# Kernel tuning notes

Measured on AMD Instinct MI355X. Metric: run time of the kernel, lower is better.

## Reference

```python
import jax, jax.numpy as jnp
import numpy as np

N = 100000      # nodes
E = 1600000     # edges (before self-loops)
FIN = 128       # in_channels
HID = 16        # hidden_channels
H = 8           # heads (layer 1)
OUT = 64        # out_channels
LN_EPS = 1e-5


def setup_inputs() -> dict:
    key = jax.random.key(0)
    ks = jax.random.split(key, 24)
    def p(i, shape):
        return jax.random.normal(ks[i], shape, dtype=jnp.float32) * 0.05
    return {
        "x": jax.random.normal(ks[0], (N, FIN), dtype=jnp.float32),
        "edge_index": jax.random.randint(ks[1], (2, E), 0, N, dtype=jnp.int32),
        # GATv2 layer 1: in -> H*HID, concat
        "Wl1": p(2, (FIN, H * HID)), "bl1": p(3, (H * HID,)),
        "Wr1": p(4, (FIN, H * HID)), "br1": p(5, (H * HID,)),
        "att1": p(6, (H, HID)), "bias1": p(7, (H * HID,)),
        # GATv2 layer 2: H*HID -> HID, heads=1
        "Wl2": p(8, (H * HID, HID)), "bl2": p(9, (HID,)),
        "Wr2": p(10, (H * HID, HID)), "br2": p(11, (HID,)),
        "att2": p(12, (1, HID)), "bias2": p(13, (HID,)),
        # LayerNorms
        "ln1_g": jnp.ones((H * HID,), jnp.float32), "ln1_b": jnp.zeros((H * HID,), jnp.float32),
        "ln2_g": jnp.ones((HID,), jnp.float32), "ln2_b": jnp.zeros((HID,), jnp.float32),
        # residual / skip / output linears
        "res1_W": p(14, (FIN, H * HID)), "res1_b": p(15, (H * HID,)),
        "res2_W": p(16, (H * HID, HID)), "res2_b": p(17, (HID,)),
        "skip_W": p(18, (H * HID, HID)), "skip_b": p(19, (HID,)),
        "out_W": p(20, (HID, OUT)), "out_b": p(21, (OUT,)),
    }


def _layernorm(x, g, b):
    mu = jnp.mean(x, axis=-1, keepdims=True)
    var = jnp.mean((x - mu) ** 2, axis=-1, keepdims=True)
    return (x - mu) * jax.lax.rsqrt(var + LN_EPS) * g + b


def _gatv2(x, src, dst, Wl, bl, Wr, br, att, bias, concat):
    # PyG GATv2Conv (share_weights=False, eval mode): message from src j to dst i
    Hh, C = att.shape
    n = x.shape[0]
    xl = (x @ Wl + bl).reshape(n, Hh, C)   # source-side transform
    xr = (x @ Wr + br).reshape(n, Hh, C)   # target-side transform
    m = xl[src] + xr[dst]                  # [E, H, C]
    e = jax.nn.leaky_relu(m, 0.2)
    alpha = jnp.einsum('ehc,hc->eh', e, att)          # [E, H]
    amax = jax.ops.segment_max(alpha, dst, num_segments=n)
    alpha = jnp.exp(alpha - amax[dst])
    denom = jax.ops.segment_sum(alpha, dst, num_segments=n)
    alpha = alpha / (denom[dst] + 1e-16)
    out = jax.ops.segment_sum(xl[src] * alpha[:, :, None], dst, num_segments=n)  # [N, H, C]
    out = out.reshape(n, Hh * C) if concat else out.mean(axis=1)
    return out + bias


def reference(x, edge_index, Wl1, bl1, Wr1, br1, att1, bias1,
              Wl2, bl2, Wr2, br2, att2, bias2,
              ln1_g, ln1_b, ln2_g, ln2_b,
              res1_W, res1_b, res2_W, res2_b, skip_W, skip_b, out_W, out_b):
    n = x.shape[0]
    loops = jnp.arange(n, dtype=edge_index.dtype)
    src = jnp.concatenate([edge_index[0], loops])
    dst = jnp.concatenate([edge_index[1], loops])

    h = _gatv2(x, src, dst, Wl1, bl1, Wr1, br1, att1, bias1, concat=True)
    h = _layernorm(h, ln1_g, ln1_b)
    h = h + (x @ res1_W + res1_b)
    h = jax.nn.elu(h)            # dropout off in eval

    skip_in = h
    h2 = _gatv2(h, src, dst, Wl2, bl2, Wr2, br2, att2, bias2, concat=False)
    h2 = _layernorm(h2, ln2_g, ln2_b)
    h2 = h2 + (skip_in @ res2_W + res2_b)
    h2 = jax.nn.elu(h2)
    h2 = h2 + (skip_in @ skip_W + skip_b)
    return h2 @ out_W + out_b
```

## Files before the change

kernel.cpp:

```cpp
#include <hip/hip_runtime.h>

typedef __attribute__((ext_vector_type(8))) short bf16x8;
typedef __attribute__((ext_vector_type(4))) float f32x4;

__device__ __forceinline__ float bf2f(ushort u) {
  union { uint i; float f; } v; v.i = ((uint)u) << 16; return v.f;
}
__device__ __forceinline__ ushort f2bf(float f) {
  union { float f; uint i; } v; v.f = f;
  uint r = (v.i + 0x7FFFu + ((v.i >> 16) & 1u)) >> 16;
  return (ushort)r;
}


__global__ __launch_bounds__(256) void k_zero(int* p, int n) {
  int i = blockIdx.x * 256 + threadIdx.x;
  if (i < n) p[i] = 0;
}

__global__ __launch_bounds__(256) void k_hist(const int* __restrict__ ei, int* __restrict__ cnt, int E) {
  int e = blockIdx.x * 256 + threadIdx.x;
  if (e < E) atomicAdd(&cnt[ei[E + e]], 1);
}

__global__ __launch_bounds__(256) void k_scan1(const int* __restrict__ cnt, int* __restrict__ partial, int n) {
  int i = blockIdx.x * 256 + threadIdx.x;
  int v = (i < n) ? cnt[i] : 0;
  #pragma unroll
  for (int m = 1; m < 64; m <<= 1) v += __shfl_xor(v, m);
  __shared__ int sm[4];
  if ((threadIdx.x & 63) == 0) sm[threadIdx.x >> 6] = v;
  __syncthreads();
  if (threadIdx.x == 0) partial[blockIdx.x] = sm[0] + sm[1] + sm[2] + sm[3];
}

__global__ __launch_bounds__(512) void k_scan2(int* partial, int nb) {
  __shared__ int buf[2][512];
  int t = threadIdx.x;
  int v = (t < nb) ? partial[t] : 0;
  buf[0][t] = v;
  __syncthreads();
  int cur = 0;
  for (int off = 1; off < 512; off <<= 1) {
    int x = buf[cur][t];
    if (t >= off) x += buf[cur][t - off];
    buf[cur ^ 1][t] = x;
    __syncthreads();
    cur ^= 1;
  }
  if (t < nb) partial[t] = buf[cur][t] - v;
}

__global__ __launch_bounds__(256) void k_scan3(const int* __restrict__ cnt, const int* __restrict__ partial,
                                               int* __restrict__ rowptr, int* __restrict__ cursor, int n) {
  __shared__ int buf[2][256];
  int t = threadIdx.x;
  int i = blockIdx.x * 256 + t;
  int v = (i < n) ? cnt[i] : 0;
  buf[0][t] = v;
  __syncthreads();
  int cur = 0;
  for (int off = 1; off < 256; off <<= 1) {
    int x = buf[cur][t];
    if (t >= off) x += buf[cur][t - off];
    buf[cur ^ 1][t] = x;
    __syncthreads();
    cur ^= 1;
  }
  if (i < n) {
    int incl = buf[cur][t];
    int base = partial[blockIdx.x];
    int rp = base + incl - v;
    rowptr[i] = rp;
    cursor[i] = rp;
    if (i == n - 1) rowptr[n] = base + incl;
  }
}

__global__ __launch_bounds__(256) void k_scatter(const int* __restrict__ ei, int* __restrict__ cursor,
                                                 int* __restrict__ ssrc, int E, int NS) {
  int t = threadIdx.x;
  int base = blockIdx.x * 2048;
  int src[8], dst[8];
  #pragma unroll
  for (int j = 0; j < 8; ++j) {
    int idx = base + j * 256 + t;
    bool ok = idx < E;
    src[j] = ok ? ei[idx] : 0;
    dst[j] = ok ? ei[E + idx] : -1;
  }
  for (int s = 0; s < NS; ++s) {
    #pragma unroll
    for (int j = 0; j < 8; ++j) {
      if ((dst[j] >> 13) == s) {
        int pos = atomicAdd(&cursor[dst[j]], 1);
        ssrc[pos] = src[j];
      }
    }
  }
}


__global__ __launch_bounds__(256) void k_conv(const float* __restrict__ x, ushort* __restrict__ AF, int total) {
  int t = blockIdx.x * 256 + threadIdx.x;
  if (t >= total) return;
  int m = t >> 4, k8 = t & 15;
  const float* src = x + (size_t)m * 128 + k8 * 8;
  float4 f0 = *(const float4*)src;
  float4 f1 = *(const float4*)(src + 4);
  uint4 o;
  o.x = f2bf(f0.x) | ((uint)f2bf(f0.y) << 16);
  o.y = f2bf(f0.z) | ((uint)f2bf(f0.w) << 16);
  o.z = f2bf(f1.x) | ((uint)f2bf(f1.y) << 16);
  o.w = f2bf(f1.z) | ((uint)f2bf(f1.w) << 16);
  size_t off = ((size_t)(((m >> 4) * 4 + (k8 >> 2)) * 64) + (m & 15) + ((k8 & 3) << 4)) * 8;
  *(uint4*)(AF + off) = o;
}


__global__ __launch_bounds__(256) void k_pack(
    const float* __restrict__ Wl1, const float* __restrict__ bl1,
    const float* __restrict__ Wr1, const float* __restrict__ br1,
    const float* __restrict__ res1W, const float* __restrict__ res1b,
    const float* __restrict__ Wl2, const float* __restrict__ bl2,
    const float* __restrict__ Wr2, const float* __restrict__ br2,
    const float* __restrict__ res2W, const float* __restrict__ res2b,
    const float* __restrict__ skipW, const float* __restrict__ skipb,
    ushort* __restrict__ W1F, float* __restrict__ B1P,
    ushort* __restrict__ W2F, float* __restrict__ B2P) {
  int tid = blockIdx.x * 256 + threadIdx.x;
  if (tid < 49152) {
    int j = tid & 7, l = (tid >> 3) & 63, ktile = (tid >> 9) & 3, ct = tid >> 11;
    int k = ktile * 32 + ((l >> 4) << 3) + j;
    int n = ct * 16 + (l & 15);
    int sel = n >> 7, jj = n & 127;
    const float* s = sel == 0 ? Wl1 : sel == 1 ? Wr1 : res1W;
    W1F[tid] = f2bf(s[k * 128 + jj]);
  } else if (tid < 57344) {
    int u = tid - 49152;
    int j = u & 7, l = (u >> 3) & 63, ktile = (u >> 9) & 3, ct = u >> 11;
    int k = ktile * 32 + ((l >> 4) << 3) + j;
    int n = ct * 16 + (l & 15);
    int sel = n >> 4, jj = n & 15;
    const float* s = sel == 0 ? Wl2 : sel == 1 ? Wr2 : sel == 2 ? res2W : skipW;
    W2F[u] = f2bf(s[k * 16 + jj]);
  } else if (tid < 57728) {
    int n = tid - 57344;
    int sel = n >> 7, jj = n & 127;
    const float* sb = sel == 0 ? bl1 : sel == 1 ? br1 : res1b;
    B1P[n] = sb[jj];
  } else if (tid < 57792) {
    int n = tid - 57728;
    int sel = n >> 4, jj = n & 15;
    const float* sb = sel == 0 ? bl2 : sel == 1 ? br2 : sel == 2 ? res2b : skipb;
    B2P[n] = sb[jj];
  }
}


__global__ __launch_bounds__(256) void k_mfma(
    const ushort* __restrict__ AF, const ushort* __restrict__ WF,
    const float* __restrict__ bias, ushort* __restrict__ C, int M, int P) {
  int w = threadIdx.x >> 6, l = threadIdx.x & 63;
  int m0 = blockIdx.x * 64;
  int c0 = blockIdx.y * 64 + w * 16;
  int ct = c0 >> 4;
  f32x4 acc[4] = {};
  #pragma unroll
  for (int kt = 0; kt < 4; ++kt) {
    bf16x8 b = *(const bf16x8*)(WF + ((size_t)((ct * 4 + kt) * 64 + l)) * 8);
    #pragma unroll
    for (int rt = 0; rt < 4; ++rt) {
      bf16x8 a = *(const bf16x8*)(AF + ((size_t)((blockIdx.x * 16 + rt * 4 + kt) * 64 + l)) * 8);
      acc[rt] = __builtin_amdgcn_mfma_f32_16x16x32_bf16(a, b, acc[rt], 0, 0, 0);
    }
  }
  int col = c0 + (l & 15);
  float bv = bias[col];
  int rbase = m0 + ((l >> 4) << 2);
  #pragma unroll
  for (int rt = 0; rt < 4; ++rt) {
    #pragma unroll
    for (int r = 0; r < 4; ++r) {
      int m = rbase + rt * 16 + r;
      if (m < M) C[(size_t)m * P + col] = f2bf(acc[rt][r] + bv);
    }
  }
}


__device__ __forceinline__ float2 ld2bf(const ushort* p) {
  uint u = *(const uint*)p;
  return make_float2(bf2f((ushort)u), bf2f((ushort)(u >> 16)));
}

#define EDGE1(v)                                            \
  {                                                         \
    float mx = (v).x + xr.x, my = (v).y + xr.y;             \
    mx = mx > 0.f ? mx : 0.2f * mx;                         \
    my = my > 0.f ? my : 0.2f * my;                         \
    float tt = mx * atv.x + my * atv.y;                     \
    tt += __shfl_xor(tt, 1);                                \
    tt += __shfl_xor(tt, 2);                                \
    tt += __shfl_xor(tt, 4);                                \
    float p = __expf(tt);                                   \
    accx += p * (v).x; accy += p * (v).y; den += p;         \
  }

__global__ __launch_bounds__(256) void k_gat1(
    const ushort* __restrict__ X,
    const float* __restrict__ att, const float* __restrict__ bias1,
    const float* __restrict__ g1, const float* __restrict__ b1,
    const int* __restrict__ rowptr, const int* __restrict__ ssrc,
    ushort* __restrict__ HF, int n) {
  int lane = threadIdx.x & 63;
  int i = blockIdx.x * 4 + (threadIdx.x >> 6);
  if (i >= n) return;
  int f = lane * 2;
  const ushort* rowi = X + (size_t)i * 384;
  float2 xl_self = ld2bf(rowi + f);
  float2 xr = ld2bf(rowi + 128 + f);
  float2 atv = *(const float2*)&att[f];
  float accx = 0.f, accy = 0.f, den = 0.f;
  EDGE1(xl_self);
  int e0 = rowptr[i], e1 = rowptr[i + 1];
  for (int base = e0; base < e1; base += 64) {
    int cnt = e1 - base; if (cnt > 64) cnt = 64;
    int sidx = (lane < cnt) ? ssrc[base + lane] : 0;
    int j = 0;
    for (; j + 4 <= cnt; j += 4) {
      int s0 = __shfl(sidx, j);
      int s1 = __shfl(sidx, j + 1);
      int s2 = __shfl(sidx, j + 2);
      int s3 = __shfl(sidx, j + 3);
      float2 v0 = ld2bf(X + (size_t)s0 * 384 + f);
      float2 v1 = ld2bf(X + (size_t)s1 * 384 + f);
      float2 v2 = ld2bf(X + (size_t)s2 * 384 + f);
      float2 v3 = ld2bf(X + (size_t)s3 * 384 + f);
      EDGE1(v0); EDGE1(v1); EDGE1(v2); EDGE1(v3);
    }
    for (; j < cnt; ++j) {
      int s = __shfl(sidx, j);
      float2 v = ld2bf(X + (size_t)s * 384 + f);
      EDGE1(v);
    }
  }
  float inv = 1.f / (den + 1e-16f);
  float2 bv = *(const float2*)&bias1[f];
  float ox = accx * inv + bv.x, oy = accy * inv + bv.y;
  float s = ox + oy;
  #pragma unroll
  for (int m = 1; m < 64; m <<= 1) s += __shfl_xor(s, m);
  float mu = s * (1.f / 128.f);
  float dx = ox - mu, dy = oy - mu;
  float q = dx * dx + dy * dy;
  #pragma unroll
  for (int m = 1; m < 64; m <<= 1) q += __shfl_xor(q, m);
  float rstd = rsqrtf(q * (1.f / 128.f) + 1e-5f);
  float2 gg = *(const float2*)&g1[f];
  float2 bb = *(const float2*)&b1[f];
  float2 rv = ld2bf(rowi + 256 + f);
  float yx = dx * rstd * gg.x + bb.x + rv.x;
  float yy = dy * rstd * gg.y + bb.y + rv.y;
  yx = yx > 0.f ? yx : __expf(yx) - 1.f;
  yy = yy > 0.f ? yy : __expf(yy) - 1.f;
  size_t off = (((size_t)(i >> 4) * 4 + (lane >> 4)) * 64 + (i & 15) + ((lane >> 2) & 3) * 16) * 8
               + 2 * (lane & 3);
  *(uint*)(HF + off) = (uint)f2bf(yx) | ((uint)f2bf(yy) << 16);
}


#define EDGE2(v)                                            \
  {                                                         \
    float m = (v) + xr; m = m > 0.f ? m : 0.2f * m;         \
    float tt = m * a2;                                      \
    tt += __shfl_xor(tt, 1);                                \
    tt += __shfl_xor(tt, 2);                                \
    tt += __shfl_xor(tt, 4);                                \
    tt += __shfl_xor(tt, 8);                                \
    float p = __expf(tt);                                   \
    acc += p * (v); den += p;                               \
  }

__global__ __launch_bounds__(256) void k_gat2(
    const ushort* __restrict__ XC, const float* __restrict__ att2,
    const float* __restrict__ bias2,
    const float* __restrict__ g2, const float* __restrict__ b2,
    const int* __restrict__ rowptr, const int* __restrict__ ssrc,
    const float* __restrict__ outW, const float* __restrict__ outB,
    float* __restrict__ Out, int n) {
  __shared__ float sW[1024];
  __shared__ float sB[64];
  int t = threadIdx.x;
  for (int idx = t; idx < 1024; idx += 256) sW[idx] = outW[idx];
  if (t < 64) sB[t] = outB[t];
  __syncthreads();
  int c = t & 15;
  int i = blockIdx.x * 16 + (t >> 4);
  if (i >= n) return;
  const ushort* row = XC + (size_t)i * 64;
  float xl = bf2f(row[c]), xr = bf2f(row[16 + c]);
  float resv = bf2f(row[32 + c]), skipv = bf2f(row[48 + c]);
  float a2 = att2[c];
  float acc = 0.f, den = 0.f;
  EDGE2(xl);
  int e0 = rowptr[i], e1 = rowptr[i + 1];
  for (int base = e0; base < e1; base += 16) {
    int cnt = e1 - base; if (cnt > 16) cnt = 16;
    int sidx = (c < cnt) ? ssrc[base + c] : 0;
    int j = 0;
    for (; j + 4 <= cnt; j += 4) {
      int s0 = __shfl(sidx, j, 16);
      int s1 = __shfl(sidx, j + 1, 16);
      int s2 = __shfl(sidx, j + 2, 16);
      int s3 = __shfl(sidx, j + 3, 16);
      float v0 = bf2f(XC[(size_t)s0 * 64 + c]);
      float v1 = bf2f(XC[(size_t)s1 * 64 + c]);
      float v2 = bf2f(XC[(size_t)s2 * 64 + c]);
      float v3 = bf2f(XC[(size_t)s3 * 64 + c]);
      EDGE2(v0); EDGE2(v1); EDGE2(v2); EDGE2(v3);
    }
    for (; j < cnt; ++j) {
      int s = __shfl(sidx, j, 16);
      float v = bf2f(XC[(size_t)s * 64 + c]);
      EDGE2(v);
    }
  }
  float o = acc / (den + 1e-16f) + bias2[c];
  float s = o;
  #pragma unroll
  for (int m = 1; m < 16; m <<= 1) s += __shfl_xor(s, m);
  float mu = s * (1.f / 16.f);
  float d = o - mu;
  float q = d * d;
  #pragma unroll
  for (int m = 1; m < 16; m <<= 1) q += __shfl_xor(q, m);
  float rstd = rsqrtf(q * (1.f / 16.f) + 1e-5f);
  float y = d * rstd * g2[c] + b2[c] + resv;
  y = y > 0.f ? y : __expf(y) - 1.f;
  y += skipv;
  float a0 = sB[c * 4 + 0], a1 = sB[c * 4 + 1], ao2 = sB[c * 4 + 2], a3 = sB[c * 4 + 3];
  #pragma unroll
  for (int cc = 0; cc < 16; ++cc) {
    float h = __shfl(y, cc, 16);
    a0 += h * sW[cc * 64 + c * 4 + 0];
    a1 += h * sW[cc * 64 + c * 4 + 1];
    ao2 += h * sW[cc * 64 + c * 4 + 2];
    a3 += h * sW[cc * 64 + c * 4 + 3];
  }
  *(float4*)&Out[(size_t)i * 64 + c * 4] = make_float4(a0, a1, ao2, a3);
}


extern "C" void kernel_launch(void* const* d_in, const int* in_sizes, int n_in,
                              void* d_out, int out_size, void* d_ws, size_t ws_size,
                              hipStream_t stream) {
  const float* x     = (const float*)d_in[0];
  const int*   ei    = (const int*)d_in[1];
  const float* Wl1   = (const float*)d_in[2];
  const float* bl1   = (const float*)d_in[3];
  const float* Wr1   = (const float*)d_in[4];
  const float* br1   = (const float*)d_in[5];
  const float* att1  = (const float*)d_in[6];
  const float* bias1 = (const float*)d_in[7];
  const float* Wl2   = (const float*)d_in[8];
  const float* bl2   = (const float*)d_in[9];
  const float* Wr2   = (const float*)d_in[10];
  const float* br2   = (const float*)d_in[11];
  const float* att2  = (const float*)d_in[12];
  const float* bias2 = (const float*)d_in[13];
  const float* ln1g  = (const float*)d_in[14];
  const float* ln1b  = (const float*)d_in[15];
  const float* ln2g  = (const float*)d_in[16];
  const float* ln2b  = (const float*)d_in[17];
  const float* res1W = (const float*)d_in[18];
  const float* res1b = (const float*)d_in[19];
  const float* res2W = (const float*)d_in[20];
  const float* res2b = (const float*)d_in[21];
  const float* skipW = (const float*)d_in[22];
  const float* skipb = (const float*)d_in[23];
  const float* outW  = (const float*)d_in[24];
  const float* outb  = (const float*)d_in[25];
  int N = in_sizes[0] / 128;
  int E = in_sizes[1] / 2;
  float* out = (float*)d_out;

  int nblk = (N + 63) / 64;
  int ngrp = nblk * 4;

  ushort* XF   = (ushort*)d_ws;
  ushort* XLRR = XF + (size_t)ngrp * 2048;
  ushort* HF   = XLRR + (size_t)N * 384;
  ushort* XC   = HF + (size_t)ngrp * 2048;
  ushort* W1F  = XC + (size_t)N * 64;
  ushort* W2F  = W1F + 49152;
  float*  B1P  = (float*)(W2F + 8192);
  float*  B2P  = B1P + 384;
  int* cnt     = (int*)(B2P + 64);
  int* cursor  = cnt + N;
  int* rowptr  = cursor + N;
  int* ssrc    = rowptr + N + 1;
  int* partial = ssrc + E;

  int nbS = (N + 255) / 256;
  int nbE = (E + 255) / 256;
  int NS = ((N - 1) >> 13) + 1;

  k_pack<<<226, 256, 0, stream>>>(Wl1, bl1, Wr1, br1, res1W, res1b,
                                  Wl2, bl2, Wr2, br2, res2W, res2b, skipW, skipb,
                                  W1F, B1P, W2F, B2P);
  k_conv<<<(N * 16 + 255) / 256, 256, 0, stream>>>(x, XF, N * 16);

  k_zero<<<nbS, 256, 0, stream>>>(cnt, N);
  k_hist<<<nbE, 256, 0, stream>>>(ei, cnt, E);
  k_scan1<<<nbS, 256, 0, stream>>>(cnt, partial, N);
  k_scan2<<<1, 512, 0, stream>>>(partial, nbS);
  k_scan3<<<nbS, 256, 0, stream>>>(cnt, partial, rowptr, cursor, N);
  k_scatter<<<(E + 2047) / 2048, 256, 0, stream>>>(ei, cursor, ssrc, E, NS);

  dim3 g1g(nblk, 6);
  k_mfma<<<g1g, 256, 0, stream>>>(XF, W1F, B1P, XLRR, N, 384);

  k_gat1<<<(N + 3) / 4, 256, 0, stream>>>(XLRR, att1, bias1, ln1g, ln1b,
                                          rowptr, ssrc, HF, N);

  dim3 g2g(nblk, 1);
  k_mfma<<<g2g, 256, 0, stream>>>(HF, W2F, B2P, XC, N, 64);
  k_gat2<<<(N + 15) / 16, 256, 0, stream>>>(XC, att2, bias2, ln2g, ln2b,
                                            rowptr, ssrc, outW, outb, out, N);
}
```

Before: 506.9 us.

## Split projection outputs into separate arrays and streamline edge softmax inner loops

The GEMM epilogue now writes the source, target, residual and skip projections into separate contiguous arrays, so the gathered source rows are compact (128 or 16 elements per row instead of 384 or 64). The edge loops compute leaky-ReLU as 0.6*x+0.4*|x|, fold log2(e) into precomputed attention vectors so exp2 can be used, replace shuffle reductions with DPP adds, and use readlane/readfirstlane for broadcast indices. In layer 2, each lane now reads the source indices directly instead of staging and shuffling them. The aim is to cut gather bandwidth and ALU/LDS-permute cost in the edge-bound kernels, at the cost of more arrays and some reliance on DPP row semantics.

```diff
diff --git a/kernel.cpp b/kernel.cpp
--- a/kernel.cpp
+++ b/kernel.cpp
@@ -11,6 +11,18 @@
   uint r = (v.i + 0x7FFFu + ((v.i >> 16) & 1u)) >> 16;
   return (ushort)r;
 }
+
+template <int CTRL>
+__device__ __forceinline__ float dppadd(float x) {
+  union { float f; int i; } a, b;
+  a.f = x;
+  b.i = __builtin_amdgcn_update_dpp(0, a.i, CTRL, 0xF, 0xF, true);
+  return a.f + b.f;
+}
+#define DPP_X1 0xB1
+#define DPP_X2 0x4E
+#define DPP_X7 0x141
+#define DPP_XF 0x140
 
 
 __global__ __launch_bounds__(256) void k_zero(int* p, int n) {
@@ -126,8 +138,11 @@
     const float* __restrict__ Wr2, const float* __restrict__ br2,
     const float* __restrict__ res2W, const float* __restrict__ res2b,
     const float* __restrict__ skipW, const float* __restrict__ skipb,
+    const float* __restrict__ att1, const float* __restrict__ att2,
     ushort* __restrict__ W1F, float* __restrict__ B1P,
-    ushort* __restrict__ W2F, float* __restrict__ B2P) {
+    ushort* __restrict__ W2F, float* __restrict__ B2P,
+    float* __restrict__ attE, float* __restrict__ at2E) {
+  const float LOG2E = 1.4426950408889634f;
   int tid = blockIdx.x * 256 + threadIdx.x;
   if (tid < 49152) {
     int j = tid & 7, l = (tid >> 3) & 63, ktile = (tid >> 9) & 3, ct = tid >> 11;
@@ -154,13 +169,22 @@
     int sel = n >> 4, jj = n & 15;
     const float* sb = sel == 0 ? bl2 : sel == 1 ? br2 : sel == 2 ? res2b : skipb;
     B2P[n] = sb[jj];
+  } else if (tid < 57920) {
+    int n = tid - 57792;
+    attE[n] = att1[n] * LOG2E;
+  } else if (tid < 57936) {
+    int n = tid - 57920;
+    at2E[n] = att2[n] * LOG2E;
   }
 }
 
 
 __global__ __launch_bounds__(256) void k_mfma(
     const ushort* __restrict__ AF, const ushort* __restrict__ WF,
-    const float* __restrict__ bias, ushort* __restrict__ C, int M, int P) {
+    const float* __restrict__ bias,
+    ushort* __restrict__ O0, ushort* __restrict__ O1,
+    ushort* __restrict__ O2, ushort* __restrict__ O3,
+    int M, int cs_shift) {
   int w = threadIdx.x >> 6, l = threadIdx.x & 63;
   int m0 = blockIdx.x * 64;
   int c0 = blockIdx.y * 64 + w * 16;
@@ -176,6 +200,10 @@
     }
   }
   int col = c0 + (l & 15);
+  int arr = col >> cs_shift;
+  ushort* O = arr == 0 ? O0 : arr == 1 ? O1 : arr == 2 ? O2 : O3;
+  int stride = 1 << cs_shift;
+  int lcol = col & (stride - 1);
   float bv = bias[col];
   int rbase = m0 + ((l >> 4) << 2);
   #pragma unroll
@@ -183,33 +211,31 @@
     #pragma unroll
     for (int r = 0; r < 4; ++r) {
       int m = rbase + rt * 16 + r;
-      if (m < M) C[(size_t)m * P + col] = f2bf(acc[rt][r] + bv);
+      if (m < M) O[(size_t)m * stride + lcol] = f2bf(acc[rt][r] + bv);
     }
   }
 }
 
 
-__device__ __forceinline__ float2 ld2bf(const ushort* p) {
-  uint u = *(const uint*)p;
-  return make_float2(bf2f((ushort)u), bf2f((ushort)(u >> 16)));
-}
-
-#define EDGE1(v)                                            \
-  {                                                         \
-    float mx = (v).x + xr.x, my = (v).y + xr.y;             \
-    mx = mx > 0.f ? mx : 0.2f * mx;                         \
-    my = my > 0.f ? my : 0.2f * my;                         \
-    float tt = mx * atv.x + my * atv.y;                     \
-    tt += __shfl_xor(tt, 1);                                \
-    tt += __shfl_xor(tt, 2);                                \
-    tt += __shfl_xor(tt, 4);                                \
-    float p = __expf(tt);                                   \
-    accx += p * (v).x; accy += p * (v).y; den += p;         \
+#define EDGE1U(u)                                                          \
+  {                                                                        \
+    float vx = __builtin_bit_cast(float, (u) << 16);                       \
+    float vy = __builtin_bit_cast(float, (u) & 0xffff0000u);               \
+    float mx = vx + xr.x, my = vy + xr.y;                                  \
+    float ta = atv.x * mx + atv.y * my;                                    \
+    float tb = atv.x * __builtin_fabsf(mx) + atv.y * __builtin_fabsf(my);  \
+    float tt = 0.6f * ta + 0.4f * tb;                                      \
+    tt = dppadd<DPP_X1>(tt);                                               \
+    tt = dppadd<DPP_X2>(tt);                                               \
+    tt = dppadd<DPP_X7>(tt);                                               \
+    float p = __builtin_amdgcn_exp2f(tt);                                  \
+    accx += p * vx; accy += p * vy; den += p;                              \
   }
 
 __global__ __launch_bounds__(256) void k_gat1(
-    const ushort* __restrict__ X,
-    const float* __restrict__ att, const float* __restrict__ bias1,
+    const ushort* __restrict__ XLG, const ushort* __restrict__ XR,
+    const ushort* __restrict__ RE,
+    const float* __restrict__ attE, const float* __restrict__ bias1,
     const float* __restrict__ g1, const float* __restrict__ b1,
     const int* __restrict__ rowptr, const int* __restrict__ ssrc,
     ushort* __restrict__ HF, int n) {
@@ -217,32 +243,36 @@
   int i = blockIdx.x * 4 + (threadIdx.x >> 6);
   if (i >= n) return;
   int f = lane * 2;
-  const ushort* rowi = X + (size_t)i * 384;
-  float2 xl_self = ld2bf(rowi + f);
-  float2 xr = ld2bf(rowi + 128 + f);
-  float2 atv = *(const float2*)&att[f];
+  size_t ib = (size_t)i << 7;
+  uint u_self = *(const uint*)(XLG + ib + f);
+  float2 xr;
+  { uint u = *(const uint*)(XR + ib + f);
+    xr = make_float2(__builtin_bit_cast(float, u << 16),
+                     __builtin_bit_cast(float, u & 0xffff0000u)); }
+  float2 atv = *(const float2*)&attE[f];
   float accx = 0.f, accy = 0.f, den = 0.f;
-  EDGE1(xl_self);
-  int e0 = rowptr[i], e1 = rowptr[i + 1];
+  EDGE1U(u_self);
+  int e0 = __builtin_amdgcn_readfirstlane(rowptr[i]);
+  int e1 = __builtin_amdgcn_readfirstlane(rowptr[i + 1]);
   for (int base = e0; base < e1; base += 64) {
     int cnt = e1 - base; if (cnt > 64) cnt = 64;
-    int sidx = (lane < cnt) ? ssrc[base + lane] : 0;
+    int sidx = ssrc[base + (lane < cnt ? lane : cnt - 1)];
     int j = 0;
     for (; j + 4 <= cnt; j += 4) {
-      int s0 = __shfl(sidx, j);
-      int s1 = __shfl(sidx, j + 1);
-      int s2 = __shfl(sidx, j + 2);
-      int s3 = __shfl(sidx, j + 3);
-      float2 v0 = ld2bf(X + (size_t)s0 * 384 + f);
-      float2 v1 = ld2bf(X + (size_t)s1 * 384 + f);
-      float2 v2 = ld2bf(X + (size_t)s2 * 384 + f);
-      float2 v3 = ld2bf(X + (size_t)s3 * 384 + f);
-      EDGE1(v0); EDGE1(v1); EDGE1(v2); EDGE1(v3);
+      int s0 = __builtin_amdgcn_readlane(sidx, j);
+      int s1 = __builtin_amdgcn_readlane(sidx, j + 1);
+      int s2 = __builtin_amdgcn_readlane(sidx, j + 2);
+      int s3 = __builtin_amdgcn_readlane(sidx, j + 3);
+      uint u0 = *(const uint*)(XLG + ((size_t)(uint)s0 << 7) + f);
+      uint u1 = *(const uint*)(XLG + ((size_t)(uint)s1 << 7) + f);
+      uint u2 = *(const uint*)(XLG + ((size_t)(uint)s2 << 7) + f);
+      uint u3 = *(const uint*)(XLG + ((size_t)(uint)s3 << 7) + f);
+      EDGE1U(u0); EDGE1U(u1); EDGE1U(u2); EDGE1U(u3);
     }
     for (; j < cnt; ++j) {
-      int s = __shfl(sidx, j);
-      float2 v = ld2bf(X + (size_t)s * 384 + f);
-      EDGE1(v);
+      int s = __builtin_amdgcn_readlane(sidx, j);
+      uint u = *(const uint*)(XLG + ((size_t)(uint)s << 7) + f);
+      EDGE1U(u);
     }
   }
   float inv = 1.f / (den + 1e-16f);
@@ -259,7 +289,10 @@
   float rstd = rsqrtf(q * (1.f / 128.f) + 1e-5f);
   float2 gg = *(const float2*)&g1[f];
   float2 bb = *(const float2*)&b1[f];
-  float2 rv = ld2bf(rowi + 256 + f);
+  float2 rv;
+  { uint u = *(const uint*)(RE + ib + f);
+    rv = make_float2(__builtin_bit_cast(float, u << 16),
+                     __builtin_bit_cast(float, u & 0xffff0000u)); }
   float yx = dx * rstd * gg.x + bb.x + rv.x;
   float yy = dy * rstd * gg.y + bb.y + rv.y;
   yx = yx > 0.f ? yx : __expf(yx) - 1.f;
@@ -270,21 +303,24 @@
 }
 
 
-#define EDGE2(v)                                            \
-  {                                                         \
-    float m = (v) + xr; m = m > 0.f ? m : 0.2f * m;         \
-    float tt = m * a2;                                      \
-    tt += __shfl_xor(tt, 1);                                \
-    tt += __shfl_xor(tt, 2);                                \
-    tt += __shfl_xor(tt, 4);                                \
-    tt += __shfl_xor(tt, 8);                                \
-    float p = __expf(tt);                                   \
-    acc += p * (v); den += p;                               \
+#define EDGE2V(v)                                            \
+  {                                                          \
+    float m = (v) + xr;                                      \
+    float ta = a2 * m;                                       \
+    float tb = a2 * __builtin_fabsf(m);                      \
+    float tt = 0.6f * ta + 0.4f * tb;                        \
+    tt = dppadd<DPP_X1>(tt);                                 \
+    tt = dppadd<DPP_X2>(tt);                                 \
+    tt = dppadd<DPP_X7>(tt);                                 \
+    tt = dppadd<DPP_XF>(tt);                                 \
+    float p = __builtin_amdgcn_exp2f(tt);                    \
+    acc += p * (v); den += p;                                \
   }
 
 __global__ __launch_bounds__(256) void k_gat2(
-    const ushort* __restrict__ XC, const float* __restrict__ att2,
-    const float* __restrict__ bias2,
+    const ushort* __restrict__ XG, const ushort* __restrict__ XRr,
+    const ushort* __restrict__ XE, const ushort* __restrict__ XS,
+    const float* __restrict__ at2E, const float* __restrict__ bias2,
     const float* __restrict__ g2, const float* __restrict__ b2,
     const int* __restrict__ rowptr, const int* __restrict__ ssrc,
     const float* __restrict__ outW, const float* __restrict__ outB,
@@ -298,43 +334,34 @@
   int c = t & 15;
   int i = blockIdx.x * 16 + (t >> 4);
   if (i >= n) return;
-  const ushort* row = XC + (size_t)i * 64;
-  float xl = bf2f(row[c]), xr = bf2f(row[16 + c]);
-  float resv = bf2f(row[32 + c]), skipv = bf2f(row[48 + c]);
-  float a2 = att2[c];
+  size_t ib = (size_t)i << 4;
+  float xl = bf2f(XG[ib + c]), xr = bf2f(XRr[ib + c]);
+  float resv = bf2f(XE[ib + c]), skipv = bf2f(XS[ib + c]);
+  float a2 = at2E[c];
   float acc = 0.f, den = 0.f;
-  EDGE2(xl);
+  EDGE2V(xl);
   int e0 = rowptr[i], e1 = rowptr[i + 1];
-  for (int base = e0; base < e1; base += 16) {
-    int cnt = e1 - base; if (cnt > 16) cnt = 16;
-    int sidx = (c < cnt) ? ssrc[base + c] : 0;
-    int j = 0;
-    for (; j + 4 <= cnt; j += 4) {
-      int s0 = __shfl(sidx, j, 16);
-      int s1 = __shfl(sidx, j + 1, 16);
-      int s2 = __shfl(sidx, j + 2, 16);
-      int s3 = __shfl(sidx, j + 3, 16);
-      float v0 = bf2f(XC[(size_t)s0 * 64 + c]);
-      float v1 = bf2f(XC[(size_t)s1 * 64 + c]);
-      float v2 = bf2f(XC[(size_t)s2 * 64 + c]);
-      float v3 = bf2f(XC[(size_t)s3 * 64 + c]);
-      EDGE2(v0); EDGE2(v1); EDGE2(v2); EDGE2(v3);
-    }
-    for (; j < cnt; ++j) {
-      int s = __shfl(sidx, j, 16);
-      float v = bf2f(XC[(size_t)s * 64 + c]);
-      EDGE2(v);
-    }
+  int e = e0;
+  for (; e + 4 <= e1; e += 4) {
+    int s0 = ssrc[e], s1 = ssrc[e + 1], s2 = ssrc[e + 2], s3 = ssrc[e + 3];
+    float v0 = bf2f(XG[((size_t)(uint)s0 << 4) + c]);
+    float v1 = bf2f(XG[((size_t)(uint)s1 << 4) + c]);
+    float v2 = bf2f(XG[((size_t)(uint)s2 << 4) + c]);
+    float v3 = bf2f(XG[((size_t)(uint)s3 << 4) + c]);
+    EDGE2V(v0); EDGE2V(v1); EDGE2V(v2); EDGE2V(v3);
+  }
+  for (; e < e1; ++e) {
+    int s = ssrc[e];
+    float v = bf2f(XG[((size_t)(uint)s << 4) + c]);
+    EDGE2V(v);
   }
   float o = acc / (den + 1e-16f) + bias2[c];
   float s = o;
-  #pragma unroll
-  for (int m = 1; m < 16; m <<= 1) s += __shfl_xor(s, m);
+  s = dppadd<DPP_X1>(s); s = dppadd<DPP_X2>(s); s = dppadd<DPP_X7>(s); s = dppadd<DPP_XF>(s);
   float mu = s * (1.f / 16.f);
   float d = o - mu;
   float q = d * d;
-  #pragma unroll
-  for (int m = 1; m < 16; m <<= 1) q += __shfl_xor(q, m);
+  q = dppadd<DPP_X1>(q); q = dppadd<DPP_X2>(q); q = dppadd<DPP_X7>(q); q = dppadd<DPP_XF>(q);
   float rstd = rsqrtf(q * (1.f / 16.f) + 1e-5f);
   float y = d * rstd * g2[c] + b2[c] + resv;
   y = y > 0.f ? y : __expf(y) - 1.f;
@@ -389,14 +416,21 @@
   int ngrp = nblk * 4;
 
   ushort* XF   = (ushort*)d_ws;
-  ushort* XLRR = XF + (size_t)ngrp * 2048;
-  ushort* HF   = XLRR + (size_t)N * 384;
-  ushort* XC   = HF + (size_t)ngrp * 2048;
-  ushort* W1F  = XC + (size_t)N * 64;
+  ushort* XLG  = XF + (size_t)ngrp * 2048;
+  ushort* XR1  = XLG + (size_t)N * 128;
+  ushort* RE1  = XR1 + (size_t)N * 128;
+  ushort* HF   = RE1 + (size_t)N * 128;
+  ushort* XG2  = HF + (size_t)ngrp * 2048;
+  ushort* X2R  = XG2 + (size_t)N * 16;
+  ushort* X2E  = X2R + (size_t)N * 16;
+  ushort* X2S  = X2E + (size_t)N * 16;
+  ushort* W1F  = X2S + (size_t)N * 16;
   ushort* W2F  = W1F + 49152;
   float*  B1P  = (float*)(W2F + 8192);
   float*  B2P  = B1P + 384;
-  int* cnt     = (int*)(B2P + 64);
+  float*  attE = B2P + 64;
+  float*  at2E = attE + 128;
+  int* cnt     = (int*)(at2E + 16);
   int* cursor  = cnt + N;
   int* rowptr  = cursor + N;
   int* ssrc    = rowptr + N + 1;
@@ -406,9 +440,9 @@
   int nbE = (E + 255) / 256;
   int NS = ((N - 1) >> 13) + 1;
 
-  k_pack<<<226, 256, 0, stream>>>(Wl1, bl1, Wr1, br1, res1W, res1b,
+  k_pack<<<227, 256, 0, stream>>>(Wl1, bl1, Wr1, br1, res1W, res1b,
                                   Wl2, bl2, Wr2, br2, res2W, res2b, skipW, skipb,
-                                  W1F, B1P, W2F, B2P);
+                                  att1, att2, W1F, B1P, W2F, B2P, attE, at2E);
   k_conv<<<(N * 16 + 255) / 256, 256, 0, stream>>>(x, XF, N * 16);
 
   k_zero<<<nbS, 256, 0, stream>>>(cnt, N);
@@ -419,13 +453,13 @@
   k_scatter<<<(E + 2047) / 2048, 256, 0, stream>>>(ei, cursor, ssrc, E, NS);
 
   dim3 g1g(nblk, 6);
-  k_mfma<<<g1g, 256, 0, stream>>>(XF, W1F, B1P, XLRR, N, 384);
-
-  k_gat1<<<(N + 3) / 4, 256, 0, stream>>>(XLRR, att1, bias1, ln1g, ln1b,
+  k_mfma<<<g1g, 256, 0, stream>>>(XF, W1F, B1P, XLG, XR1, RE1, XLG, N, 7);
+
+  k_gat1<<<(N + 3) / 4, 256, 0, stream>>>(XLG, XR1, RE1, attE, bias1, ln1g, ln1b,
                                           rowptr, ssrc, HF, N);
 
   dim3 g2g(nblk, 1);
-  k_mfma<<<g2g, 256, 0, stream>>>(HF, W2F, B2P, XC, N, 64);
-  k_gat2<<<(N + 15) / 16, 256, 0, stream>>>(XC, att2, bias2, ln2g, ln2b,
+  k_mfma<<<g2g, 256, 0, stream>>>(HF, W2F, B2P, XG2, X2R, X2E, X2S, N, 4);
+  k_gat2<<<(N + 15) / 16, 256, 0, stream>>>(XG2, X2R, X2E, X2S, at2E, bias2, ln2g, ln2b,
                                             rowptr, ssrc, outW, outb, out, N);
 }
```

Result: faster. 487.6 us (-3.8%).
